# Optimization experiments

Measured on AMD Instinct MI355X. Metric: run time of the kernel, lower is better.

Reference implementation:

```python
import jax, jax.numpy as jnp
import numpy as np

NEG_INF = -1e9  # same masked_fill constant as the torch module
ALPHA = 0.1     # LeakyReLU negative slope


def setup_inputs() -> dict:
    key = jax.random.key(0)
    k1, k2, k3, k4, k5 = jax.random.split(key, 5)
    B, N, Din, Dout = 8, 2048, 512, 512
    features = jax.random.normal(k1, (B, N, Din), dtype=jnp.float32)
    graph = jax.random.randint(k2, (B, N, N), 0, 2, dtype=jnp.int64)
    # xavier_uniform with gain=1.414: limit = gain*sqrt(6/(fan_in+fan_out))
    lim_w = 1.414 * np.sqrt(6.0 / (Din + Dout))
    w = jax.random.uniform(k3, (Din, Dout), jnp.float32, -lim_w, lim_w)
    lim_a = 1.414 * np.sqrt(6.0 / (Dout + 1))
    a1 = jax.random.uniform(k4, (Dout, 1), jnp.float32, -lim_a, lim_a)
    a2 = jax.random.uniform(k5, (Dout, 1), jnp.float32, -lim_a, lim_a)
    return {"features": features, "graph": graph, "w": w, "a1": a1, "a2": a2}


def reference(features, graph, w, a1, a2):
    # hidden: [B, N, Dout]
    hidden = jnp.einsum("bni,io->bno", features, w)
    s1 = hidden @ a1  # [B, N, 1] -> broadcasts over columns
    s2 = hidden @ a2  # [B, N, 1] -> transposed broadcasts over rows
    # e[b,i,j] = leaky_relu(s1[b,i] + s2[b,j])
    e = jax.nn.leaky_relu(s1 + jnp.swapaxes(s2, 1, 2), negative_slope=ALPHA)
    e = jnp.where(graph == 0, NEG_INF, e)
    attn = jax.nn.softmax(e, axis=-1)  # [B, N, N]; dropout p=0 -> identity
    h_prime = jnp.einsum("bij,bjo->bio", attn, hidden)
    return jax.nn.elu(h_prime)  # concat=True
```

## Files before the change

kernel.cpp:

```cpp
#include <hip/hip_runtime.h>
#include <math.h>

#define B_ 8
#define N_ 2048
#define D_ 512
#define NROWS (B_ * N_)
#define NEG_ALPHA 0.1f

typedef __bf16 bf16;
typedef __bf16 bf16x4 __attribute__((ext_vector_type(4)));
typedef __bf16 bf16x8 __attribute__((ext_vector_type(8)));
typedef float f32x4 __attribute__((ext_vector_type(4)));
typedef float f32x16 __attribute__((ext_vector_type(16)));

__global__ __launch_bounds__(256) void k_prep(const float* __restrict__ W,
                                              bf16* __restrict__ Wt) {
  const int dout = blockIdx.x;
  const int t = threadIdx.x;
#pragma unroll
  for (int p = 0; p < 2; ++p) {
    int din = t + p * 256;
    Wt[dout * D_ + din] = (bf16)W[din * D_ + dout];
  }
}

__global__ __launch_bounds__(256) void k_wa(const float* __restrict__ W,
                                            const float* __restrict__ a1,
                                            const float* __restrict__ a2,
                                            float* __restrict__ wa1,
                                            float* __restrict__ wa2) {
  const int wv = threadIdx.x >> 6, lane = threadIdx.x & 63;
  const int row = blockIdx.x * 4 + wv;
  const float* wr = W + (size_t)row * D_;
  float d1 = 0.f, d2 = 0.f;
#pragma unroll
  for (int p = 0; p < 8; ++p) {
    int c = lane + p * 64;
    float w = wr[c];
    d1 = fmaf(w, a1[c], d1);
    d2 = fmaf(w, a2[c], d2);
  }
#pragma unroll
  for (int off = 32; off > 0; off >>= 1) {
    d1 += __shfl_down(d1, off, 64);
    d2 += __shfl_down(d2, off, 64);
  }
  if (lane == 0) {
    wa1[row] = d1;
    wa2[row] = d2;
  }
}

__global__ __launch_bounds__(256) void k_scores_x(const float* __restrict__ X,
                                                  const float* __restrict__ wa1,
                                                  const float* __restrict__ wa2,
                                                  float* __restrict__ s1,
                                                  float* __restrict__ s2) {
  const int wv = threadIdx.x >> 6, lane = threadIdx.x & 63;
  const int r = blockIdx.x * 4 + wv;
  const float* x = X + (size_t)r * D_;
  float d1 = 0.f, d2 = 0.f;
#pragma unroll
  for (int p = 0; p < 2; ++p) {
    int c = lane * 4 + p * 256;
    float4 xv = *(const float4*)&x[c];
    float4 w1 = *(const float4*)&wa1[c];
    float4 w2 = *(const float4*)&wa2[c];
    d1 += xv.x * w1.x + xv.y * w1.y + xv.z * w1.z + xv.w * w1.w;
    d2 += xv.x * w2.x + xv.y * w2.y + xv.z * w2.z + xv.w * w2.w;
  }
#pragma unroll
  for (int off = 32; off > 0; off >>= 1) {
    d1 += __shfl_down(d1, off, 64);
    d2 += __shfl_down(d2, off, 64);
  }
  if (lane == 0) {
    s1[r] = d1;
    s2[r] = d2;
  }
}

#define LDH 40

__global__ __launch_bounds__(256, 2) void k_hiddenT(const float* __restrict__ X,
                                                    const bf16* __restrict__ Wt,
                                                    bf16* __restrict__ Ht) {
  __shared__ bf16 As[128][LDH];
  __shared__ bf16 Bs[128][LDH];
  const int t = threadIdx.x;
  const int m0 = blockIdx.y * 128;
  const int n0 = blockIdx.x * 128;
  const int lane = t & 63, w = t >> 6;
  const int wm = w >> 1, wn = w & 1;
  const int l15 = lane & 15, q = lane >> 4;

  f32x4 acc[4][4];
#pragma unroll
  for (int i = 0; i < 4; ++i)
#pragma unroll
    for (int j = 0; j < 4; ++j) acc[i][j] = (f32x4){0.f, 0.f, 0.f, 0.f};

  bf16x8 av[2];
  float4 bv[4];
#pragma unroll
  for (int p = 0; p < 2; ++p) {
    int s = t + p * 256;
    av[p] = *(const bf16x8*)&Wt[(size_t)(m0 + (s >> 2)) * D_ + (s & 3) * 8];
  }
#pragma unroll
  for (int p = 0; p < 4; ++p) {
    int s = t + p * 256;
    bv[p] = *(const float4*)&X[(size_t)(n0 + (s >> 3)) * D_ + (s & 7) * 4];
  }

  for (int k0 = 0; k0 < D_; k0 += 32) {
    __syncthreads();
#pragma unroll
    for (int p = 0; p < 2; ++p) {
      int s = t + p * 256;
      *(bf16x8*)&As[s >> 2][(s & 3) * 8] = av[p];
    }
#pragma unroll
    for (int p = 0; p < 4; ++p) {
      int s = t + p * 256;
      float4 v = bv[p];
      bf16x4 h = {(bf16)v.x, (bf16)v.y, (bf16)v.z, (bf16)v.w};
      *(bf16x4*)&Bs[s >> 3][(s & 7) * 4] = h;
    }
    __syncthreads();
    if (k0 + 32 < D_) {
#pragma unroll
      for (int p = 0; p < 2; ++p) {
        int s = t + p * 256;
        av[p] = *(const bf16x8*)&Wt[(size_t)(m0 + (s >> 2)) * D_ + k0 + 32 + (s & 3) * 8];
      }
#pragma unroll
      for (int p = 0; p < 4; ++p) {
        int s = t + p * 256;
        bv[p] = *(const float4*)&X[(size_t)(n0 + (s >> 3)) * D_ + k0 + 32 + (s & 7) * 4];
      }
    }
    bf16x8 a[4], bb[4];
#pragma unroll
    for (int i = 0; i < 4; ++i)
      a[i] = *(const bf16x8*)&As[wm * 64 + i * 16 + l15][q * 8];
#pragma unroll
    for (int j = 0; j < 4; ++j)
      bb[j] = *(const bf16x8*)&Bs[wn * 64 + j * 16 + l15][q * 8];
#pragma unroll
    for (int i = 0; i < 4; ++i)
#pragma unroll
      for (int j = 0; j < 4; ++j)
        acc[i][j] =
            __builtin_amdgcn_mfma_f32_16x16x32_bf16(a[i], bb[j], acc[i][j], 0, 0, 0);
  }
#pragma unroll
  for (int i = 0; i < 4; ++i)
#pragma unroll
    for (int r = 0; r < 4; ++r) {
      int dout = m0 + wm * 64 + i * 16 + q * 4 + r;
#pragma unroll
      for (int j = 0; j < 4; ++j) {
        int row = n0 + wn * 64 + j * 16 + l15;
        Ht[(size_t)dout * NROWS + row] = (bf16)acc[i][j][r];
      }
    }
}

#define AT_BM 64
#define AT_BK 64
#define LDP 72

__global__ __launch_bounds__(512, 1) void k_attn(const bf16* __restrict__ Ht,
                                                 const int* __restrict__ graph,
                                                 const float* __restrict__ s1,
                                                 const float* __restrict__ s2,
                                                 float* __restrict__ out) {
  __shared__ bf16 Hs[D_][LDP];
  __shared__ bf16 Ps[AT_BM][LDP];
  __shared__ float s2s[N_];
  __shared__ float sum_part[AT_BM][8];
  __shared__ float row_sum[AT_BM];

  const int t = threadIdx.x;
  const int b = blockIdx.y;
  const int i0 = blockIdx.x * AT_BM;
  const int lane = t & 63, w = t >> 6;
  const int r31 = lane & 31, half = lane >> 5;

  const bf16* Htb = Ht + (size_t)b * N_;
  const int* Gb = graph + ((size_t)b * N_ + i0) * N_;

  for (int c = t; c < N_; c += 512) s2s[c] = s2[b * N_ + c];

  const int pi = t >> 3;
  const int pj = (t & 7) * 8;
  const float s1r = s1[b * N_ + i0 + pi];
  float rsum = 0.f;

  f32x16 acc[2][2];
#pragma unroll
  for (int i = 0; i < 2; ++i)
#pragma unroll
    for (int j = 0; j < 2; ++j)
#pragma unroll
      for (int r = 0; r < 16; ++r) acc[i][j][r] = 0.f;

  bf16x8 hv[8];
  int4 g0, g1;
#pragma unroll
  for (int p = 0; p < 8; ++p) {
    int s = t + p * 512;
    hv[p] = *(const bf16x8*)&Htb[(size_t)(s >> 3) * NROWS + (s & 7) * 8];
  }
  g0 = *(const int4*)&Gb[(size_t)pi * N_ + pj];
  g1 = *(const int4*)&Gb[(size_t)pi * N_ + pj + 4];

  __syncthreads();

  for (int j0 = 0; j0 < N_; j0 += AT_BK) {
    float pv[8];
    {
      int gg[8] = {g0.x, g0.y, g0.z, g0.w, g1.x, g1.y, g1.z, g1.w};
#pragma unroll
      for (int q = 0; q < 8; ++q) {
        float e = s1r + s2s[j0 + pj + q];
        e = (e > 0.f) ? e : NEG_ALPHA * e;
        pv[q] = (gg[q] != 0) ? __expf(e) : 0.f;
        rsum += pv[q];
      }
    }
    __syncthreads();
#pragma unroll
    for (int p = 0; p < 8; ++p) {
      int s = t + p * 512;
      *(bf16x8*)&Hs[s >> 3][(s & 7) * 8] = hv[p];
    }
    {
      bf16x8 pb = {(bf16)pv[0], (bf16)pv[1], (bf16)pv[2], (bf16)pv[3],
                   (bf16)pv[4], (bf16)pv[5], (bf16)pv[6], (bf16)pv[7]};
      *(bf16x8*)&Ps[pi][pj] = pb;
    }
    __syncthreads();
    if (j0 + AT_BK < N_) {
#pragma unroll
      for (int p = 0; p < 8; ++p) {
        int s = t + p * 512;
        hv[p] = *(const bf16x8*)&Htb[(size_t)(s >> 3) * NROWS + j0 + AT_BK + (s & 7) * 8];
      }
      g0 = *(const int4*)&Gb[(size_t)pi * N_ + j0 + AT_BK + pj];
      g1 = *(const int4*)&Gb[(size_t)pi * N_ + j0 + AT_BK + pj + 4];
    }
#pragma unroll
    for (int ks = 0; ks < 4; ++ks) {
      const int ko = ks * 16 + half * 8;
      bf16x8 a0 = *(const bf16x8*)&Ps[r31][ko];
      bf16x8 a1 = *(const bf16x8*)&Ps[32 + r31][ko];
      bf16x8 b0 = *(const bf16x8*)&Hs[w * 64 + r31][ko];
      bf16x8 b1 = *(const bf16x8*)&Hs[w * 64 + 32 + r31][ko];
      acc[0][0] = __builtin_amdgcn_mfma_f32_32x32x16_bf16(a0, b0, acc[0][0], 0, 0, 0);
      acc[0][1] = __builtin_amdgcn_mfma_f32_32x32x16_bf16(a0, b1, acc[0][1], 0, 0, 0);
      acc[1][0] = __builtin_amdgcn_mfma_f32_32x32x16_bf16(a1, b0, acc[1][0], 0, 0, 0);
      acc[1][1] = __builtin_amdgcn_mfma_f32_32x32x16_bf16(a1, b1, acc[1][1], 0, 0, 0);
    }
  }

  sum_part[pi][t & 7] = rsum;
  __syncthreads();
  if (t < AT_BM) {
    float s = 0.f;
#pragma unroll
    for (int k = 0; k < 8; ++k) s += sum_part[t][k];
    row_sum[t] = s;
  }
  __syncthreads();

#pragma unroll
  for (int mt = 0; mt < 2; ++mt) {
    float inv[16];
#pragma unroll
    for (int r = 0; r < 16; ++r)
      inv[r] = 1.f / row_sum[mt * 32 + (r & 3) + 8 * (r >> 2) + 4 * half];
#pragma unroll
    for (int nt = 0; nt < 2; ++nt) {
      const int d = w * 64 + nt * 32 + r31;
#pragma unroll
      for (int r = 0; r < 16; ++r) {
        int i = mt * 32 + (r & 3) + 8 * (r >> 2) + 4 * half;
        float x = acc[mt][nt][r] * inv[r];
        out[((size_t)b * N_ + i0 + i) * D_ + d] = (x > 0.f) ? x : expm1f(x);
      }
    }
  }
}

extern "C" void kernel_launch(void* const* d_in, const int* in_sizes, int n_in,
                              void* d_out, int out_size, void* d_ws,
                              size_t ws_size, hipStream_t stream) {
  const float* X = (const float*)d_in[0];
  const int* graph = (const int*)d_in[1];
  const float* W = (const float*)d_in[2];
  const float* a1 = (const float*)d_in[3];
  const float* a2 = (const float*)d_in[4];
  float* out = (float*)d_out;

  char* ws = (char*)d_ws;
  bf16* Wt = (bf16*)ws;
  bf16* Ht = (bf16*)(ws + (1 << 19));
  float* s1 = (float*)(ws + (1 << 19) + (16 << 20));
  float* s2 = s1 + NROWS;
  float* wa1 = s2 + NROWS;
  float* wa2 = wa1 + D_;

  hipLaunchKernelGGL(k_prep, dim3(512), dim3(256), 0, stream, W, Wt);
  hipLaunchKernelGGL(k_wa, dim3(128), dim3(256), 0, stream, W, a1, a2, wa1, wa2);
  hipLaunchKernelGGL(k_scores_x, dim3(NROWS / 4), dim3(256), 0, stream, X, wa1,
                     wa2, s1, s2);
  hipLaunchKernelGGL(k_hiddenT, dim3(NROWS / 128, D_ / 128), dim3(256), 0,
                     stream, X, Wt, Ht);
  hipLaunchKernelGGL(k_attn, dim3(N_ / AT_BM, B_), dim3(512), 0, stream, Ht,
                     graph, s1, s2, out);
}
```

Before: 305.1 us.

## Stream H directly from global in attention, double-buffer P tiles, merge prep kernels

The attention kernel stops staging the hidden tile in shared memory and instead loads MFMA B operands straight from global/L2. The transposed hidden buffer gets a padded stride to avoid cache-set aliasing. The P tile is double-buffered so one barrier per chunk suffices, and the chunk size doubles to 128. Computing the next chunk's exponentials is moved after the MFMAs so it can overlap them. The two small weight-prep kernels are merged into one launch. The risk is more global-load latency on the MFMA path, since 8 waves each read their own H rows.

```diff
diff --git a/kernel.cpp b/kernel.cpp
--- a/kernel.cpp
+++ b/kernel.cpp
@@ -5,6 +5,7 @@
 #define N_ 2048
 #define D_ 512
 #define NROWS (B_ * N_)
+#define HTS (NROWS + 32)
 #define NEG_ALPHA 0.1f
 
 typedef __bf16 bf16;
@@ -13,41 +14,40 @@
 typedef float f32x4 __attribute__((ext_vector_type(4)));
 typedef float f32x16 __attribute__((ext_vector_type(16)));
 
-__global__ __launch_bounds__(256) void k_prep(const float* __restrict__ W,
-                                              bf16* __restrict__ Wt) {
-  const int dout = blockIdx.x;
+__global__ __launch_bounds__(256) void k_prep_wa(const float* __restrict__ W,
+                                                 const float* __restrict__ a1,
+                                                 const float* __restrict__ a2,
+                                                 bf16* __restrict__ Wt,
+                                                 float* __restrict__ wa1,
+                                                 float* __restrict__ wa2) {
   const int t = threadIdx.x;
+  const int bid = blockIdx.x;
 #pragma unroll
   for (int p = 0; p < 2; ++p) {
     int din = t + p * 256;
-    Wt[dout * D_ + din] = (bf16)W[din * D_ + dout];
-  }
-}
-
-__global__ __launch_bounds__(256) void k_wa(const float* __restrict__ W,
-                                            const float* __restrict__ a1,
-                                            const float* __restrict__ a2,
-                                            float* __restrict__ wa1,
-                                            float* __restrict__ wa2) {
-  const int wv = threadIdx.x >> 6, lane = threadIdx.x & 63;
-  const int row = blockIdx.x * 4 + wv;
-  const float* wr = W + (size_t)row * D_;
-  float d1 = 0.f, d2 = 0.f;
-#pragma unroll
-  for (int p = 0; p < 8; ++p) {
-    int c = lane + p * 64;
-    float w = wr[c];
-    d1 = fmaf(w, a1[c], d1);
-    d2 = fmaf(w, a2[c], d2);
-  }
-#pragma unroll
-  for (int off = 32; off > 0; off >>= 1) {
-    d1 += __shfl_down(d1, off, 64);
-    d2 += __shfl_down(d2, off, 64);
-  }
-  if (lane == 0) {
-    wa1[row] = d1;
-    wa2[row] = d2;
+    Wt[bid * D_ + din] = (bf16)W[(size_t)din * D_ + bid];
+  }
+  if (bid < 128) {
+    const int wv = t >> 6, lane = t & 63;
+    const int row = bid * 4 + wv;
+    const float* wr = W + (size_t)row * D_;
+    float d1 = 0.f, d2 = 0.f;
+#pragma unroll
+    for (int p = 0; p < 8; ++p) {
+      int c = lane + p * 64;
+      float w = wr[c];
+      d1 = fmaf(w, a1[c], d1);
+      d2 = fmaf(w, a2[c], d2);
+    }
+#pragma unroll
+    for (int off = 32; off > 0; off >>= 1) {
+      d1 += __shfl_down(d1, off, 64);
+      d2 += __shfl_down(d2, off, 64);
+    }
+    if (lane == 0) {
+      wa1[row] = d1;
+      wa2[row] = d2;
+    }
   }
 }
 
@@ -162,22 +162,22 @@
 #pragma unroll
       for (int j = 0; j < 4; ++j) {
         int row = n0 + wn * 64 + j * 16 + l15;
-        Ht[(size_t)dout * NROWS + row] = (bf16)acc[i][j][r];
+        Ht[(size_t)dout * HTS + row] = (bf16)acc[i][j][r];
       }
     }
 }
 
 #define AT_BM 64
-#define AT_BK 64
-#define LDP 72
+#define AT_BK 128
+#define NCHUNK (N_ / AT_BK)
+#define LDPS 136
 
 __global__ __launch_bounds__(512, 1) void k_attn(const bf16* __restrict__ Ht,
                                                  const int* __restrict__ graph,
                                                  const float* __restrict__ s1,
                                                  const float* __restrict__ s2,
                                                  float* __restrict__ out) {
-  __shared__ bf16 Hs[D_][LDP];
-  __shared__ bf16 Ps[AT_BM][LDP];
+  __shared__ bf16 Ps[2][AT_BM][LDPS];
   __shared__ float s2s[N_];
   __shared__ float sum_part[AT_BM][8];
   __shared__ float row_sum[AT_BM];
@@ -187,6 +187,7 @@
   const int i0 = blockIdx.x * AT_BM;
   const int lane = t & 63, w = t >> 6;
   const int r31 = lane & 31, half = lane >> 5;
+  const int d0 = w * 64;
 
   const bf16* Htb = Ht + (size_t)b * N_;
   const int* Gb = graph + ((size_t)b * N_ + i0) * N_;
@@ -194,7 +195,7 @@
   for (int c = t; c < N_; c += 512) s2s[c] = s2[b * N_ + c];
 
   const int pi = t >> 3;
-  const int pj = (t & 7) * 8;
+  const int pj = (t & 7) * 16;
   const float s1r = s1[b * N_ + i0 + pi];
   float rsum = 0.f;
 
@@ -206,63 +207,62 @@
 #pragma unroll
       for (int r = 0; r < 16; ++r) acc[i][j][r] = 0.f;
 
-  bf16x8 hv[8];
-  int4 g0, g1;
-#pragma unroll
-  for (int p = 0; p < 8; ++p) {
-    int s = t + p * 512;
-    hv[p] = *(const bf16x8*)&Htb[(size_t)(s >> 3) * NROWS + (s & 7) * 8];
-  }
-  g0 = *(const int4*)&Gb[(size_t)pi * N_ + pj];
-  g1 = *(const int4*)&Gb[(size_t)pi * N_ + pj + 4];
+  int gg[16];
+#pragma unroll
+  for (int u = 0; u < 4; ++u)
+    *(int4*)&gg[u * 4] = *(const int4*)&Gb[(size_t)pi * N_ + pj + u * 4];
 
   __syncthreads();
 
-  for (int j0 = 0; j0 < N_; j0 += AT_BK) {
-    float pv[8];
+  float pv[16];
+#pragma unroll
+  for (int u = 0; u < 16; ++u) {
+    float e = s1r + s2s[pj + u];
+    e = (e > 0.f) ? e : NEG_ALPHA * e;
+    float pe = (gg[u] != 0) ? __expf(e) : 0.f;
+    pv[u] = pe;
+    rsum += pe;
+  }
+
+  for (int p = 0; p < NCHUNK; ++p) {
+    const int j0 = p * AT_BK;
     {
-      int gg[8] = {g0.x, g0.y, g0.z, g0.w, g1.x, g1.y, g1.z, g1.w};
-#pragma unroll
-      for (int q = 0; q < 8; ++q) {
-        float e = s1r + s2s[j0 + pj + q];
-        e = (e > 0.f) ? e : NEG_ALPHA * e;
-        pv[q] = (gg[q] != 0) ? __expf(e) : 0.f;
-        rsum += pv[q];
-      }
+      bf16x8 w0 = {(bf16)pv[0], (bf16)pv[1], (bf16)pv[2], (bf16)pv[3],
+                   (bf16)pv[4], (bf16)pv[5], (bf16)pv[6], (bf16)pv[7]};
+      bf16x8 w1 = {(bf16)pv[8],  (bf16)pv[9],  (bf16)pv[10], (bf16)pv[11],
+                   (bf16)pv[12], (bf16)pv[13], (bf16)pv[14], (bf16)pv[15]};
+      *(bf16x8*)&Ps[p & 1][pi][pj] = w0;
+      *(bf16x8*)&Ps[p & 1][pi][pj + 8] = w1;
+    }
+    if (p + 1 < NCHUNK) {
+#pragma unroll
+      for (int u = 0; u < 4; ++u)
+        *(int4*)&gg[u * 4] =
+            *(const int4*)&Gb[(size_t)pi * N_ + j0 + AT_BK + pj + u * 4];
     }
     __syncthreads();
 #pragma unroll
-    for (int p = 0; p < 8; ++p) {
-      int s = t + p * 512;
-      *(bf16x8*)&Hs[s >> 3][(s & 7) * 8] = hv[p];
-    }
-    {
-      bf16x8 pb = {(bf16)pv[0], (bf16)pv[1], (bf16)pv[2], (bf16)pv[3],
-                   (bf16)pv[4], (bf16)pv[5], (bf16)pv[6], (bf16)pv[7]};
-      *(bf16x8*)&Ps[pi][pj] = pb;
-    }
-    __syncthreads();
-    if (j0 + AT_BK < N_) {
-#pragma unroll
-      for (int p = 0; p < 8; ++p) {
-        int s = t + p * 512;
-        hv[p] = *(const bf16x8*)&Htb[(size_t)(s >> 3) * NROWS + j0 + AT_BK + (s & 7) * 8];
-      }
-      g0 = *(const int4*)&Gb[(size_t)pi * N_ + j0 + AT_BK + pj];
-      g1 = *(const int4*)&Gb[(size_t)pi * N_ + j0 + AT_BK + pj + 4];
-    }
-#pragma unroll
-    for (int ks = 0; ks < 4; ++ks) {
+    for (int ks = 0; ks < 8; ++ks) {
       const int ko = ks * 16 + half * 8;
-      bf16x8 a0 = *(const bf16x8*)&Ps[r31][ko];
-      bf16x8 a1 = *(const bf16x8*)&Ps[32 + r31][ko];
-      bf16x8 b0 = *(const bf16x8*)&Hs[w * 64 + r31][ko];
-      bf16x8 b1 = *(const bf16x8*)&Hs[w * 64 + 32 + r31][ko];
+      bf16x8 b0 = *(const bf16x8*)&Htb[(size_t)(d0 + r31) * HTS + j0 + ko];
+      bf16x8 b1 = *(const bf16x8*)&Htb[(size_t)(d0 + 32 + r31) * HTS + j0 + ko];
+      bf16x8 a0 = *(const bf16x8*)&Ps[p & 1][r31][ko];
+      bf16x8 a1 = *(const bf16x8*)&Ps[p & 1][32 + r31][ko];
       acc[0][0] = __builtin_amdgcn_mfma_f32_32x32x16_bf16(a0, b0, acc[0][0], 0, 0, 0);
       acc[0][1] = __builtin_amdgcn_mfma_f32_32x32x16_bf16(a0, b1, acc[0][1], 0, 0, 0);
       acc[1][0] = __builtin_amdgcn_mfma_f32_32x32x16_bf16(a1, b0, acc[1][0], 0, 0, 0);
       acc[1][1] = __builtin_amdgcn_mfma_f32_32x32x16_bf16(a1, b1, acc[1][1], 0, 0, 0);
     }
+    if (p + 1 < NCHUNK) {
+#pragma unroll
+      for (int u = 0; u < 16; ++u) {
+        float e = s1r + s2s[j0 + AT_BK + pj + u];
+        e = (e > 0.f) ? e : NEG_ALPHA * e;
+        float pe = (gg[u] != 0) ? __expf(e) : 0.f;
+        pv[u] = pe;
+        rsum += pe;
+      }
+    }
   }
 
   sum_part[pi][t & 7] = rsum;
@@ -283,7 +283,7 @@
       inv[r] = 1.f / row_sum[mt * 32 + (r & 3) + 8 * (r >> 2) + 4 * half];
 #pragma unroll
     for (int nt = 0; nt < 2; ++nt) {
-      const int d = w * 64 + nt * 32 + r31;
+      const int d = d0 + nt * 32 + r31;
 #pragma unroll
       for (int r = 0; r < 16; ++r) {
         int i = mt * 32 + (r & 3) + 8 * (r >> 2) + 4 * half;
@@ -307,13 +307,13 @@
   char* ws = (char*)d_ws;
   bf16* Wt = (bf16*)ws;
   bf16* Ht = (bf16*)(ws + (1 << 19));
-  float* s1 = (float*)(ws + (1 << 19) + (16 << 20));
+  float* s1 = (float*)(ws + (1 << 19) + (size_t)D_ * HTS * 2);
   float* s2 = s1 + NROWS;
   float* wa1 = s2 + NROWS;
   float* wa2 = wa1 + D_;
 
-  hipLaunchKernelGGL(k_prep, dim3(512), dim3(256), 0, stream, W, Wt);
-  hipLaunchKernelGGL(k_wa, dim3(128), dim3(256), 0, stream, W, a1, a2, wa1, wa2);
+  hipLaunchKernelGGL(k_prep_wa, dim3(512), dim3(256), 0, stream, W, a1, a2, Wt,
+                     wa1, wa2);
   hipLaunchKernelGGL(k_scores_x, dim3(NROWS / 4), dim3(256), 0, stream, X, wa1,
                      wa2, s1, s2);
   hipLaunchKernelGGL(k_hiddenT, dim3(NROWS / 128, D_ / 128), dim3(256), 0,
```

Result: slower. 324.7 us (+6.4%).
